# Kernel optimization log

Hardware: AMD Instinct MI355X
Metric: run time of the kernel (lower is better)

The kernel has to match this reference:

```python
import jax, jax.numpy as jnp
import numpy as np

C = 16
STRIDES = (8, 16, 32, 64, 128)
LVL_HW = ((256, 256), (128, 128), (64, 64), (32, 32), (16, 16))
K_POS = 256
K_HN = 2048
IOU_THRESH = 0.6
EPS = 1e-8


def _cross(a, b):
    return a[..., 0] * b[..., 1] - a[..., 1] * b[..., 0]


def _grid_points():
    # MlvlPointGenerator with offset=0.5: (x+0.5)*stride, row-major (y outer)
    pts, scl = [], []
    for lvl, ((h, w), s) in enumerate(zip(LVL_HW, STRIDES)):
        xs = (jnp.arange(w, dtype=jnp.float32) + 0.5) * s
        ys = (jnp.arange(h, dtype=jnp.float32) + 0.5) * s
        yy, xx = jnp.meshgrid(ys, xs, indexing='ij')
        pts.append(jnp.stack([xx.reshape(-1), yy.reshape(-1)], -1))
        scl.append(jnp.full((h * w,), float(lvl), dtype=jnp.float32))
    return jnp.concatenate(pts, 0), jnp.concatenate(scl, 0)


def _convert(cls_l, box_l, ang_l, ctr_l):
    B = cls_l[0].shape[0]
    cls = jnp.concatenate([x.transpose(0, 2, 3, 1).reshape(B, -1, C) for x in cls_l], 1).reshape(-1, C)
    box = jnp.concatenate([jnp.concatenate([b, a], 1).transpose(0, 2, 3, 1).reshape(B, -1, 5)
                           for b, a in zip(box_l, ang_l)], 1).reshape(-1, 5)
    ctr = jnp.concatenate([x.transpose(0, 2, 3, 1).reshape(B, -1, 1) for x in ctr_l], 1).reshape(-1, 1)
    return cls, box, ctr


def _decode(points, pred):  # DistanceAnglePointCoder.decode, angle_version='le90'
    l, t, r, b, a = [pred[..., i] for i in range(5)]
    ca, sa = jnp.cos(a), jnp.sin(a)
    w, h = l + r, t + b
    oxl, oyl = (r - l) * 0.5, (b - t) * 0.5
    ox = ca * oxl - sa * oyl
    oy = sa * oxl + ca * oyl
    an = (a + jnp.pi / 2) % jnp.pi - jnp.pi / 2
    return jnp.stack([points[..., 0] + ox, points[..., 1] + oy, w, h, an], -1)


def _encode(points, gt):  # DistanceAnglePointCoder.encode
    cx, cy, w, h, a = [gt[..., i] for i in range(5)]
    ca, sa = jnp.cos(a), jnp.sin(a)
    dx, dy = points[..., 0] - cx, points[..., 1] - cy
    ox = ca * dx + sa * dy
    oy = -sa * dx + ca * dy
    return jnp.stack([w / 2 + ox, h / 2 + oy, w / 2 - ox, h / 2 - oy, a], -1)


def _inside_mask(points, boxes):  # [M,2],[P,5] -> [M,P]
    cx, cy, w, h, a = [boxes[:, i][None, :] for i in range(5)]
    ca, sa = jnp.cos(a), jnp.sin(a)
    dx = points[:, 0:1] - cx
    dy = points[:, 1:2] - cy
    ox = ca * dx + sa * dy
    oy = -sa * dx + ca * dy
    m = jnp.minimum(jnp.minimum(w / 2 + ox, w / 2 - ox), jnp.minimum(h / 2 + oy, h / 2 - oy))
    return m > 0


def _corners(boxes):  # [N,5] -> [N,4,2]
    cx, cy, w, h, a = [boxes[:, i:i + 1] for i in range(5)]
    ca, sa = jnp.cos(a), jnp.sin(a)
    dx = jnp.array([-0.5, 0.5, 0.5, -0.5], jnp.float32) * w
    dy = jnp.array([-0.5, -0.5, 0.5, 0.5], jnp.float32) * h
    return jnp.stack([cx + dx * ca - dy * sa, cy + dx * sa + dy * ca], -1)


def _inter_area(ca, cb):  # intersection area of two convex quads [4,2],[4,2]
    pa, pb = ca, cb
    da = jnp.roll(ca, -1, 0) - ca
    db = jnp.roll(cb, -1, 0) - cb
    diff = pb[None, :] - pa[:, None]                     # [4,4,2]
    den = _cross(da[:, None], db[None, :])               # [4,4]
    dsafe = jnp.where(jnp.abs(den) < 1e-10, 1.0, den)
    t = _cross(diff, db[None, :]) / dsafe
    u = _cross(diff, da[:, None]) / dsafe
    ok = (jnp.abs(den) > 1e-10) & (t >= 0) & (t <= 1) & (u >= 0) & (u <= 1)
    ipts = pa[:, None] + t[..., None] * da[:, None]

    def inside(p, c):
        e = jnp.roll(c, -1, 0) - c
        s = _cross(e[None, :], p[:, None] - c[None, :])  # [4 pts, 4 edges]
        return jnp.all(s >= -1e-9, 1) | jnp.all(s <= 1e-9, 1)

    pts = jnp.concatenate([ipts.reshape(16, 2), ca, cb], 0)   # [24,2]
    val = jnp.concatenate([ok.reshape(16), inside(ca, cb), inside(cb, ca)], 0)
    n = val.sum()
    ctr = (pts * val[:, None]).sum(0) / jnp.maximum(n, 1)
    pts = jnp.where(val[:, None], pts, ctr)  # invalid pts collapse to centroid (zero area)
    order = jnp.argsort(jnp.arctan2(pts[:, 1] - ctr[1], pts[:, 0] - ctr[0]))
    pts = pts[order]
    area = 0.5 * jnp.abs(jnp.sum(_cross(pts - ctr, jnp.roll(pts, -1, 0) - ctr)))
    return jnp.where(n >= 3, area, 0.0)


def _rotated_iou(b1, b2):  # box_iou_rotated: [M,5],[P,5] -> [M,P]
    c1, c2 = _corners(b1), _corners(b2)
    inter = jax.vmap(lambda x: jax.vmap(lambda y: _inter_area(x, y))(c2))(c1)
    a1 = jnp.abs(b1[:, 2] * b1[:, 3])
    a2 = jnp.abs(b2[:, 2] * b2[:, 3])
    return inter / (a1[:, None] + a2[None, :] - inter + EPS)


def _bce(p, t):
    p = jnp.clip(p, 1e-12, 1.0 - 1e-12)
    return -(t * jnp.log(p) + (1.0 - t) * jnp.log1p(-p))


def _smooth_l1(x, y):  # nn.SmoothL1Loss(reduction='none'), beta=1
    d = jnp.abs(x - y)
    return jnp.where(d < 1.0, 0.5 * d * d, d - 0.5)


def _arsl_loss(t_cls, t_box, t_iou, s_cls, s_box, s_iou):
    # --- teacher targets (torch.no_grad) ---
    t_cls = jax.lax.stop_gradient(t_cls)
    t_box = jax.lax.stop_gradient(t_box)
    t_iou = jax.lax.stop_gradient(t_iou)
    points, scales = _grid_points()
    N = t_cls.shape[0]
    joint = jax.nn.sigmoid(t_cls) * jax.nn.sigmoid(t_iou)   # [N,C]
    max_vals = joint.max(-1)
    class_ind = joint.argmax(-1)
    cand = max_vals >= 0.1
    n_cand = cand.sum()
    mean = jnp.sum(max_vals * cand) / jnp.maximum(n_cand, 1)
    var = jnp.sum(cand * (max_vals - mean) ** 2) / jnp.maximum(n_cand - 1, 1)  # unbiased std
    pos_thresh = jnp.minimum(mean + jnp.sqrt(var), 0.4)
    pos_thresh = jnp.where(n_cand > 0, pos_thresh, jnp.inf)
    pos_mask = max_vals >= pos_thresh
    hn_mask = cand & (max_vals < pos_thresh)
    # fallback: top-10 positives when thresholding yields none
    fb = jnp.zeros((N,), bool).at[jax.lax.top_k(max_vals, 10)[1]].set(True)
    pos_mask = jnp.where(pos_mask.any(), pos_mask, fb)

    sig_t_cls = jax.nn.sigmoid(t_cls)
    sig_t_iou = jax.nn.sigmoid(t_iou[:, 0])
    cls_targets = jnp.where((pos_mask | hn_mask)[:, None], sig_t_cls, 0.0)
    loc_targets = jnp.where(pos_mask[:, None], t_box, 0.0)
    iou_targets = jnp.where(pos_mask, sig_t_iou, 0.0)
    loc_mask = pos_mask.astype(jnp.float32)

    # --- hard negative mining (fixed-capacity top-k selection) ---
    pv, pidx = jax.lax.top_k(jnp.where(pos_mask, max_vals, -1.0), K_POS)
    p_valid = jnp.take(pos_mask, pidx)
    _, hidx = jax.lax.top_k(jnp.where(hn_mask, max_vals, -1.0), K_HN)
    h_valid = jnp.take(hn_mask, hidx)
    pos_bbox = _decode(points[pidx], t_box[pidx])
    hn_pts = points[hidx]
    hn_bbox = _decode(hn_pts, t_box[hidx])
    iou = _rotated_iou(hn_bbox, pos_bbox)                    # [K_HN, K_POS]
    scale_flag = jnp.abs(scales[pidx][None, :] - scales[hidx][:, None]) <= 1.0
    class_flag = class_ind[pidx][None, :] == class_ind[hidx][:, None]
    inside_flag = _inside_mask(hn_pts, pos_bbox)
    valid = (iou >= IOU_THRESH) & class_flag & inside_flag & scale_flag & h_valid[:, None] & p_valid[None, :]
    iou_m = jnp.where(valid, iou, 0.0)
    potential = iou_m.max(-1) > 0.0                          # [K_HN]
    w = jnp.where(valid, pv[None, :], 0.0)                   # pos joint-confidence weights
    agg_bbox = (w[..., None] * pos_bbox[None]).sum(1) / jnp.maximum(w.sum(1), EPS)[:, None]
    agg_ltrba = _encode(hn_pts, agg_bbox)
    loc_targets = loc_targets.at[hidx].set(jnp.where(potential[:, None], agg_ltrba, loc_targets[hidx]))
    loc_mask = loc_mask.at[hidx].set(jnp.where(potential, 1.0, loc_mask[hidx]))

    loc_pos = loc_mask > 0.0
    iou_targets = jnp.where(loc_pos, sig_t_iou, iou_targets)
    cls_t_max = cls_targets.max(-1)
    cls_avg = jnp.sum(cls_t_max * pos_mask)
    loc_w = jnp.where(loc_pos, cls_t_max, 0.0)
    loc_avg = loc_w.sum()
    iou_avg = loc_pos.sum()

    # --- student losses ---
    s_cls_sig = jax.nn.sigmoid(s_cls)
    s_iou_sig = jax.nn.sigmoid(s_iou)
    jc = s_cls_sig * s_iou_sig  # quality focal loss on joint confidence, gamma=2
    loss_cls = jnp.sum(_bce(jc, cls_targets) * jnp.abs(jc - cls_targets) ** 2) / jnp.maximum(cls_avg, EPS)
    loss_iou = jnp.sum(_bce(s_iou_sig[:, 0], iou_targets) * loc_pos) / jnp.maximum(iou_avg, 1)
    loss_box = jnp.sum(_smooth_l1(s_box, loc_targets) * loc_w[:, None]) / jnp.maximum(loc_avg, EPS)
    return jnp.stack([loss_cls, loss_box, loss_iou])


def setup_inputs():
    key = jax.random.key(0)
    ks = jax.random.split(key, 10)
    inp = {}
    k = 0
    for pre in ('t', 's'):
        for i, (h, w) in enumerate(LVL_HW):
            k4 = jax.random.split(ks[k], 4); k += 1
            # sparse teacher/student confidences; positive box distances in image units
            inp[f'{pre}_cls_{i}'] = jax.random.normal(k4[0], (1, C, h, w), jnp.float32) * 3.0 - 12.0
            inp[f'{pre}_box_{i}'] = jax.random.uniform(k4[1], (1, 4, h, w), jnp.float32) * 64.0 + 1.0
            inp[f'{pre}_ang_{i}'] = jax.random.normal(k4[2], (1, 1, h, w), jnp.float32) * 0.5
            inp[f'{pre}_ctr_{i}'] = jax.random.normal(k4[3], (1, 1, h, w), jnp.float32)
    return inp


def reference(t_cls_0, t_cls_1, t_cls_2, t_cls_3, t_cls_4,
              t_box_0, t_box_1, t_box_2, t_box_3, t_box_4,
              t_ang_0, t_ang_1, t_ang_2, t_ang_3, t_ang_4,
              t_ctr_0, t_ctr_1, t_ctr_2, t_ctr_3, t_ctr_4,
              s_cls_0, s_cls_1, s_cls_2, s_cls_3, s_cls_4,
              s_box_0, s_box_1, s_box_2, s_box_3, s_box_4,
              s_ang_0, s_ang_1, s_ang_2, s_ang_3, s_ang_4,
              s_ctr_0, s_ctr_1, s_ctr_2, s_ctr_3, s_ctr_4):
    t = _convert([t_cls_0, t_cls_1, t_cls_2, t_cls_3, t_cls_4],
                 [t_box_0, t_box_1, t_box_2, t_box_3, t_box_4],
                 [t_ang_0, t_ang_1, t_ang_2, t_ang_3, t_ang_4],
                 [t_ctr_0, t_ctr_1, t_ctr_2, t_ctr_3, t_ctr_4])
    s = _convert([s_cls_0, s_cls_1, s_cls_2, s_cls_3, s_cls_4],
                 [s_box_0, s_box_1, s_box_2, s_box_3, s_box_4],
                 [s_ang_0, s_ang_1, s_ang_2, s_ang_3, s_ang_4],
                 [s_ctr_0, s_ctr_1, s_ctr_2, s_ctr_3, s_ctr_4])
    return _arsl_loss(t[0], t[1], t[2], s[0], s[1], s[2])
```

## Files before the change

kernel.cpp:

```cpp
#include <hip/hip_runtime.h>
#include <math.h>

#define NPTS 87296
#define NCLS 16
#define KPOS 256
#define KHN  2048
#define TILES 341
#define CAP  4096
#define PI_F   3.14159265358979323846f
#define HPI_F  1.57079632679489661923f

struct InPtrs { const float* p[40]; };

__device__ float g_max_vals[NPTS];
__device__ float g_sig_tiou[NPTS];
__device__ float g_sig_cls_max[NPTS];
__device__ int   g_class_ind[NPTS];
__device__ int   g_pos_mask[NPTS];
__device__ int   g_hn_mask[NPTS];
__device__ int   g_hnflag[NPTS];
__device__ float g_loc_targets[NPTS * 5];
__device__ float g_bsum[TILES];
__device__ float g_bsumsq[TILES];
__device__ int   g_bcnt[TILES];
__device__ int   g_bpos[TILES];
__device__ int   g_bhn[TILES];
__device__ float g_thresh;
__device__ int   g_tp, g_thn, g_slow;
__device__ int   g_pos_cand[CAP];
__device__ int   g_hn_cand[CAP];
__device__ int   g_pidx[KPOS];
__device__ int   g_pvalid[KPOS];
__device__ float g_pv[KPOS];
__device__ int   g_hidx[KHN];
__device__ int   g_hvalid[KHN];
__device__ float g_pos_bbox[KPOS * 5];
__device__ float g_pos_cor[KPOS * 8];
__device__ float g_pos_area[KPOS];
__device__ float g_pos_scale[KPOS];
__device__ int   g_pos_class[KPOS];
__device__ float g_hn_px[KHN];
__device__ float g_hn_py[KHN];
__device__ float g_hn_cor[KHN * 8];
__device__ float g_hn_area[KHN];
__device__ float g_hn_scale[KHN];
__device__ int   g_hn_class[KHN];
__device__ float g_partials[TILES * 6];

__device__ __forceinline__ float sigmoidf(float x) {
  if (x >= 0.f) return 1.f / (1.f + expf(-x));
  float e = expf(x);
  return e / (1.f + e);
}
__device__ __forceinline__ float crs(float ax, float ay, float bx, float by) {
  return ax * by - ay * bx;
}
__device__ __forceinline__ float mod_pos(float x, float y) {
  float r = fmodf(x, y);
  if (r < 0.f) r += y;
  return r;
}
__device__ __forceinline__ float pseudo_ang(float dx, float dy) {
  float den = fabsf(dx) + fabsf(dy);
  if (den == 0.f) return 0.f;
  return copysignf(1.f - dx / den, dy);
}
__device__ __forceinline__ void point_info(int n, int& lvl, int& idx, int& hw,
                                           float& px, float& py) {
  int off, wsh; float stride;
  if (n < 65536)      { lvl = 0; off = 0;     wsh = 8; stride = 8.f;   hw = 65536; }
  else if (n < 81920) { lvl = 1; off = 65536; wsh = 7; stride = 16.f;  hw = 16384; }
  else if (n < 86016) { lvl = 2; off = 81920; wsh = 6; stride = 32.f;  hw = 4096; }
  else if (n < 87040) { lvl = 3; off = 86016; wsh = 5; stride = 64.f;  hw = 1024; }
  else                { lvl = 4; off = 87040; wsh = 4; stride = 128.f; hw = 256; }
  idx = n - off;
  int y = idx >> wsh, x = idx & ((1 << wsh) - 1);
  px = ((float)x + 0.5f) * stride;
  py = ((float)y + 0.5f) * stride;
}

#define MASK_ALL 0
#define MASK_POS 1
#define MASK_HN  2
__device__ __forceinline__ int sel_mask(int mode, int n) {
  return mode == MASK_ALL ? 1 : (mode == MASK_POS ? g_pos_mask[n] : g_hn_mask[n]);
}

__device__ void radix_select_mask(int mode, int K, int* out_idx, int* out_valid, float* out_val,
                                  int* hist, int* scan_a, int* scan_b, int* sh) {
  int tid = threadIdx.x;
  int c = 0;
  for (int n = tid; n < NPTS; n += 256) if (sel_mask(mode, n)) c++;
  scan_a[tid] = c; __syncthreads();
  for (int st = 128; st > 0; st >>= 1) {
    if (tid < st) scan_a[tid] += scan_a[tid + st];
    __syncthreads();
  }
  int total = scan_a[0];
  __syncthreads();

  unsigned kth = 0u;
  if (total > K) {
    unsigned prefix = 0; int rem = K;
    for (int pass = 0; pass < 4; pass++) {
      int shift = 24 - 8 * pass;
      hist[tid] = 0;
      __syncthreads();
      for (int n = tid; n < NPTS; n += 256) {
        if (sel_mask(mode, n)) {
          unsigned k = __float_as_uint(g_max_vals[n]);
          if (pass == 0 || ((k >> (shift + 8)) == prefix))
            atomicAdd(&hist[(k >> shift) & 255], 1);
        }
      }
      __syncthreads();
      if (tid == 0) {
        int cum = 0, b = 255;
        for (; b > 0; b--) {
          if (cum + hist[b] >= rem) break;
          cum += hist[b];
        }
        sh[0] = (int)((prefix << 8) | (unsigned)b);
        sh[1] = rem - cum;
      }
      __syncthreads();
      prefix = (unsigned)sh[0]; rem = sh[1];
      __syncthreads();
    }
    kth = prefix;
  }

  const int chunk = (NPTS + 255) / 256;
  int start = tid * chunk; if (start > NPTS) start = NPTS;
  int end = start + chunk; if (end > NPTS) end = NPTS;
  int cgt = 0, ceq = 0;
  for (int n = start; n < end; n++) {
    if (sel_mask(mode, n)) {
      unsigned k = __float_as_uint(g_max_vals[n]);
      if (k > kth) cgt++;
      else if (k == kth) ceq++;
    }
  }
  scan_a[tid] = cgt; scan_b[tid] = ceq; __syncthreads();
  if (tid == 0) {
    int ag = 0, ae = 0;
    for (int i = 0; i < 256; i++) {
      int tg = scan_a[i], te = scan_b[i];
      scan_a[i] = ag; scan_b[i] = ae;
      ag += tg; ae += te;
    }
    sh[0] = ag; sh[1] = ae;
  }
  __syncthreads();
  int cnt_gt = sh[0], cnt_eq = sh[1];
  int og = scan_a[tid], oe = cnt_gt + scan_b[tid];
  for (int n = start; n < end; n++) {
    if (sel_mask(mode, n)) {
      unsigned k = __float_as_uint(g_max_vals[n]);
      if (k > kth) {
        out_idx[og] = n; out_valid[og] = 1;
        if (out_val) out_val[og] = g_max_vals[n];
        og++;
      } else if (k == kth) {
        if (oe < K) {
          out_idx[oe] = n; out_valid[oe] = 1;
          if (out_val) out_val[oe] = g_max_vals[n];
        }
        oe++;
      }
    }
  }
  int kmc = K - cnt_gt;
  int used = cnt_gt + (cnt_eq < kmc ? cnt_eq : kmc);
  __syncthreads();
  for (int i = used + tid; i < K; i += 256) {
    out_idx[i] = 0; out_valid[i] = 0;
    if (out_val) out_val[i] = -1.f;
  }
  __syncthreads();
}

__device__ void radix_select_list(const int* list, int count, int K,
                                  int* out_idx, int* out_valid, float* out_val,
                                  int* hist, int* scan_a, int* scan_b, int* sh) {
  int tid = threadIdx.x;
  unsigned prefix = 0; int rem = K;
  for (int pass = 0; pass < 4; pass++) {
    int shift = 24 - 8 * pass;
    hist[tid] = 0;
    __syncthreads();
    for (int i = tid; i < count; i += 256) {
      unsigned k = __float_as_uint(g_max_vals[list[i]]);
      if (pass == 0 || ((k >> (shift + 8)) == prefix))
        atomicAdd(&hist[(k >> shift) & 255], 1);
    }
    __syncthreads();
    if (tid == 0) {
      int cum = 0, b = 255;
      for (; b > 0; b--) {
        if (cum + hist[b] >= rem) break;
        cum += hist[b];
      }
      sh[0] = (int)((prefix << 8) | (unsigned)b);
      sh[1] = rem - cum;
    }
    __syncthreads();
    prefix = (unsigned)sh[0]; rem = sh[1];
    __syncthreads();
  }
  unsigned kth = prefix;
  int chunk = (count + 255) / 256;
  int start = tid * chunk; if (start > count) start = count;
  int end = start + chunk; if (end > count) end = count;
  int cgt = 0, ceq = 0;
  for (int i = start; i < end; i++) {
    unsigned k = __float_as_uint(g_max_vals[list[i]]);
    if (k > kth) cgt++;
    else if (k == kth) ceq++;
  }
  scan_a[tid] = cgt; scan_b[tid] = ceq; __syncthreads();
  if (tid == 0) {
    int ag = 0, ae = 0;
    for (int i = 0; i < 256; i++) {
      int tg = scan_a[i], te = scan_b[i];
      scan_a[i] = ag; scan_b[i] = ae;
      ag += tg; ae += te;
    }
    sh[0] = ag;
  }
  __syncthreads();
  int cnt_gt = sh[0];
  int og = scan_a[tid], oe = cnt_gt + scan_b[tid];
  for (int i = start; i < end; i++) {
    int n = list[i];
    unsigned k = __float_as_uint(g_max_vals[n]);
    if (k > kth) {
      out_idx[og] = n; out_valid[og] = 1;
      if (out_val) out_val[og] = g_max_vals[n];
      og++;
    } else if (k == kth) {
      if (oe < K) {
        out_idx[oe] = n; out_valid[oe] = 1;
        if (out_val) out_val[oe] = g_max_vals[n];
      }
      oe++;
    }
  }
  __syncthreads();
}

__device__ void decode_box(int n, const InPtrs& P, float* bb, float* cor,
                           float& area, float& scale, int& cls_out,
                           float* opx, float* opy) {
  int lvl, idx, hw; float px, py;
  point_info(n, lvl, idx, hw, px, py);
  const float* box = P.p[lvl * 4 + 1];
  const float* ang = P.p[lvl * 4 + 2];
  float l = box[idx], t = box[hw + idx], r = box[2 * hw + idx], b = box[3 * hw + idx];
  float a = ang[idx];
  float ca = cosf(a), sa = sinf(a);
  float w = l + r, h = t + b;
  float oxl = (r - l) * 0.5f, oyl = (b - t) * 0.5f;
  float ox = ca * oxl - sa * oyl;
  float oy = sa * oxl + ca * oyl;
  float an = mod_pos(a + HPI_F, PI_F) - HPI_F;
  float cx = px + ox, cy = py + oy;
  bb[0] = cx; bb[1] = cy; bb[2] = w; bb[3] = h; bb[4] = an;
  float c2 = cosf(an), s2 = sinf(an);
  const float dxs[4] = {-0.5f, 0.5f, 0.5f, -0.5f};
  const float dys[4] = {-0.5f, -0.5f, 0.5f, 0.5f};
#pragma unroll
  for (int k = 0; k < 4; k++) {
    float dx = dxs[k] * w, dy = dys[k] * h;
    cor[2 * k]     = cx + dx * c2 - dy * s2;
    cor[2 * k + 1] = cy + dx * s2 + dy * c2;
  }
  area = fabsf(w * h);
  scale = (float)lvl;
  cls_out = g_class_ind[n];
  if (opx) { *opx = px; *opy = py; }
}

__device__ void decode_to_pos_slot(int o, int n, const InPtrs& P) {
  float bb[5], cor[8], ar, sc; int cl;
  decode_box(n, P, bb, cor, ar, sc, cl, (float*)0, (float*)0);
#pragma unroll
  for (int k = 0; k < 5; k++) g_pos_bbox[o * 5 + k] = bb[k];
#pragma unroll
  for (int k = 0; k < 8; k++) g_pos_cor[o * 8 + k] = cor[k];
  g_pos_area[o] = ar; g_pos_scale[o] = sc; g_pos_class[o] = cl;
  g_pv[o] = g_max_vals[n];
}
__device__ void decode_to_hn_slot(int o, int n, const InPtrs& P) {
  float bb[5], cor[8], ar, sc, px, py; int cl;
  decode_box(n, P, bb, cor, ar, sc, cl, &px, &py);
#pragma unroll
  for (int k = 0; k < 8; k++) g_hn_cor[o * 8 + k] = cor[k];
  g_hn_area[o] = ar; g_hn_scale[o] = sc; g_hn_class[o] = cl;
  g_hn_px[o] = px; g_hn_py[o] = py;
}

#define BPASS(KK, JJ)                                                      \
  _Pragma("unroll")                                                        \
  for (int i = 0; i < 32; i++) {                                           \
    int l = i ^ (JJ);                                                      \
    if (l > i) {                                                           \
      bool up = ((i & (KK)) == 0);                                         \
      float aa = sa_[i], ab = sa_[l];                                      \
      bool sw = up ? (aa > ab) : (aa < ab);                                \
      sa_[i] = sw ? ab : aa; sa_[l] = sw ? aa : ab;                        \
      float xi = sx_[i], xl = sx_[l];                                      \
      sx_[i] = sw ? xl : xi; sx_[l] = sw ? xi : xl;                        \
      float yi = sy_[i], yl = sy_[l];                                      \
      sy_[i] = sw ? yl : yi; sy_[l] = sw ? yi : yl;                        \
    }                                                                      \
  }

__device__ float inter_area(const float* __restrict__ A, const float* __restrict__ B) {
  float ax[4], ay[4], bx[4], by[4];
#pragma unroll
  for (int i = 0; i < 4; i++) {
    ax[i] = A[2 * i]; ay[i] = A[2 * i + 1];
    bx[i] = B[2 * i]; by[i] = B[2 * i + 1];
  }
  float dax[4], day[4], dbx[4], dby[4];
#pragma unroll
  for (int i = 0; i < 4; i++) {
    int i1 = (i + 1) & 3;
    dax[i] = ax[i1] - ax[i]; day[i] = ay[i1] - ay[i];
    dbx[i] = bx[i1] - bx[i]; dby[i] = by[i1] - by[i];
  }
  float px[24], py[24]; bool val[24];
#pragma unroll
  for (int i = 0; i < 4; i++) {
#pragma unroll
    for (int j = 0; j < 4; j++) {
      float dx = bx[j] - ax[i], dy = by[j] - ay[i];
      float den = crs(dax[i], day[i], dbx[j], dby[j]);
      float ad = fabsf(den);
      float ds = (ad < 1e-10f) ? 1.0f : den;
      float t = crs(dx, dy, dbx[j], dby[j]) / ds;
      float u = crs(dx, dy, dax[i], day[i]) / ds;
      bool ok = (ad > 1e-10f) & (t >= 0.f) & (t <= 1.f) & (u >= 0.f) & (u <= 1.f);
      int k = i * 4 + j;
      px[k] = ax[i] + t * dax[i];
      py[k] = ay[i] + t * day[i];
      val[k] = ok;
    }
  }
#pragma unroll
  for (int i = 0; i < 4; i++) {
    bool ge = true, le = true;
#pragma unroll
    for (int j = 0; j < 4; j++) {
      float s = crs(dbx[j], dby[j], ax[i] - bx[j], ay[i] - by[j]);
      ge = ge && (s >= -1e-9f);
      le = le && (s <= 1e-9f);
    }
    val[16 + i] = ge || le; px[16 + i] = ax[i]; py[16 + i] = ay[i];
  }
#pragma unroll
  for (int j = 0; j < 4; j++) {
    bool ge = true, le = true;
#pragma unroll
    for (int i = 0; i < 4; i++) {
      float s = crs(dax[i], day[i], bx[j] - ax[i], by[j] - ay[i]);
      ge = ge && (s >= -1e-9f);
      le = le && (s <= 1e-9f);
    }
    val[20 + j] = ge || le; px[20 + j] = bx[j]; py[20 + j] = by[j];
  }
  int n = 0; float sx = 0.f, sy = 0.f;
#pragma unroll
  for (int k = 0; k < 24; k++) if (val[k]) { n++; sx += px[k]; sy += py[k]; }
  float dn = (float)(n > 1 ? n : 1);
  float cx = sx / dn, cy = sy / dn;

  float sa_[32], sx_[32], sy_[32];
#pragma unroll
  for (int k = 0; k < 24; k++) {
    float X = val[k] ? px[k] : cx;
    float Y = val[k] ? py[k] : cy;
    sx_[k] = X; sy_[k] = Y;
    sa_[k] = pseudo_ang(X - cx, Y - cy);
  }
#pragma unroll
  for (int k = 24; k < 32; k++) {
    sa_[k] = __int_as_float(0x7f800000);
    sx_[k] = cx; sy_[k] = cy;
  }
  BPASS(2, 1)
  BPASS(4, 2)  BPASS(4, 1)
  BPASS(8, 4)  BPASS(8, 2)  BPASS(8, 1)
  BPASS(16, 8) BPASS(16, 4) BPASS(16, 2) BPASS(16, 1)
  BPASS(32, 16) BPASS(32, 8) BPASS(32, 4) BPASS(32, 2) BPASS(32, 1)

  float s2 = 0.f;
#pragma unroll
  for (int k = 0; k < 24; k++) {
    int k1 = (k + 1) % 24;
    s2 += crs(sx_[k] - cx, sy_[k] - cy, sx_[k1] - cx, sy_[k1] - cy);
  }
  float area = 0.5f * fabsf(s2);
  return (n >= 3) ? area : 0.f;
}

__global__ __launch_bounds__(256) void k_prep(InPtrs P) {
  int tid = threadIdx.x;
  int t = blockIdx.x;
  int n = t * 256 + tid;
  __shared__ float r0[256], r1[256], r2[256];

  int lvl, idx, hw; float px, py;
  point_info(n, lvl, idx, hw, px, py);
  const float* cls = P.p[lvl * 4 + 0];
  const float* ctr = P.p[lvl * 4 + 3];
  float stiou = sigmoidf(ctr[idx]);
  float mv = -1.f, scm = 0.f; int ci = 0;
  for (int c = 0; c < NCLS; c++) {
    float sc = sigmoidf(cls[c * hw + idx]);
    if (sc > scm) scm = sc;
    float j = sc * stiou;
    if (j > mv) { mv = j; ci = c; }
  }
  g_max_vals[n] = mv;
  g_class_ind[n] = ci;
  g_sig_tiou[n] = stiou;
  g_sig_cls_max[n] = scm;
  g_hnflag[n] = 0;
  float isc = (mv >= 0.1f) ? 1.f : 0.f;
  r0[tid] = isc; r1[tid] = isc * mv; r2[tid] = isc * mv * mv;
  __syncthreads();
  for (int st = 128; st > 0; st >>= 1) {
    if (tid < st) { r0[tid] += r0[tid + st]; r1[tid] += r1[tid + st]; r2[tid] += r2[tid + st]; }
    __syncthreads();
  }
  if (tid == 0) {
    g_bcnt[t] = (int)r0[0];
    g_bsum[t] = r1[0];
    g_bsumsq[t] = r2[0];
  }
}

__global__ __launch_bounds__(256) void k_mask() {
  int tid = threadIdx.x;
  int t = blockIdx.x;
  int n = t * 256 + tid;
  __shared__ float s1[256], s2[256];
  __shared__ int s0[256];
  int c = 0; float s = 0.f, q = 0.f;
  for (int i = tid; i < TILES; i += 256) { c += g_bcnt[i]; s += g_bsum[i]; q += g_bsumsq[i]; }
  s0[tid] = c; s1[tid] = s; s2[tid] = q; __syncthreads();
  for (int st = 128; st > 0; st >>= 1) {
    if (tid < st) { s0[tid] += s0[tid + st]; s1[tid] += s1[tid + st]; s2[tid] += s2[tid + st]; }
    __syncthreads();
  }
  int nc = s0[0]; float sum = s1[0], sumsq = s2[0];
  float mean = sum / (float)(nc > 1 ? nc : 1);
  float E = sumsq - 2.f * mean * sum + (float)nc * mean * mean;
  if (E < 0.f) E = 0.f;
  float var = E / (float)((nc - 1) > 1 ? (nc - 1) : 1);
  float th = fminf(mean + sqrtf(var), 0.4f);
  if (nc == 0) th = __int_as_float(0x7f800000);
  if (t == 0 && tid == 0) g_thresh = th;

  float v = g_max_vals[n];
  int pm = (v >= th) ? 1 : 0;
  int hm = (v >= 0.1f && v < th) ? 1 : 0;
  g_pos_mask[n] = pm; g_hn_mask[n] = hm;
  __syncthreads();
  __shared__ int t0[256], t1[256];
  t0[tid] = pm; t1[tid] = hm; __syncthreads();
  for (int st = 128; st > 0; st >>= 1) {
    if (tid < st) { t0[tid] += t0[tid + st]; t1[tid] += t1[tid + st]; }
    __syncthreads();
  }
  if (tid == 0) { g_bpos[t] = t0[0]; g_bhn[t] = t1[0]; }
}

__global__ __launch_bounds__(256) void k_compact(InPtrs P) {
  int tid = threadIdx.x;
  int t = blockIdx.x;
  int n = t * 256 + tid;
  __shared__ int si0[256], si1[256];

  int cp = 0, ch = 0;
  for (int i = tid; i < t; i += 256) { cp += g_bpos[i]; ch += g_bhn[i]; }
  si0[tid] = cp; si1[tid] = ch; __syncthreads();
  for (int st = 128; st > 0; st >>= 1) {
    if (tid < st) { si0[tid] += si0[tid + st]; si1[tid] += si1[tid + st]; }
    __syncthreads();
  }
  int poff = si0[0], hoff = si1[0];
  __syncthreads();

  int pm = g_pos_mask[n], hm = g_hn_mask[n];
  si0[tid] = pm; si1[tid] = hm; __syncthreads();
  for (int off = 1; off < 256; off <<= 1) {
    int ap = (tid >= off) ? si0[tid - off] : 0;
    int ah = (tid >= off) ? si1[tid - off] : 0;
    __syncthreads();
    si0[tid] += ap; si1[tid] += ah;
    __syncthreads();
  }
  if (pm) {
    int o = poff + si0[tid] - pm;
    if (o < CAP) g_pos_cand[o] = n;
    if (o < KPOS) decode_to_pos_slot(o, n, P);
  }
  if (hm) {
    int o = hoff + si1[tid] - hm;
    if (o < CAP) g_hn_cand[o] = n;
    if (o < KHN) decode_to_hn_slot(o, n, P);
  }
  if (t == TILES - 1 && tid == 255) {
    int tp = poff + si0[255];
    int thn = hoff + si1[255];
    g_tp = tp; g_thn = thn;
    g_slow = (tp == 0 || tp > KPOS || thn > KHN) ? 1 : 0;
  }
}

__global__ __launch_bounds__(256) void k_select(InPtrs P) {
  if (!g_slow) return;
  __shared__ int hist[256], si0[256], si1[256], sh_i[2];
  int tid = threadIdx.x;
  int tp = g_tp, thn = g_thn;
  int fallback = (tp == 0) ? 1 : 0;
  if (!fallback && tp <= KPOS) {
    for (int i = tid; i < KPOS; i += 256) {
      if (i < tp) {
        int m = g_pos_cand[i];
        g_pidx[i] = m; g_pvalid[i] = 1; g_pv[i] = g_max_vals[m];
      } else { g_pidx[i] = 0; g_pvalid[i] = 0; g_pv[i] = -1.f; }
    }
    __syncthreads();
  } else if (!fallback && tp <= CAP) {
    radix_select_list(g_pos_cand, tp, KPOS, g_pidx, g_pvalid, g_pv, hist, si0, si1, sh_i);
  } else if (!fallback) {
    radix_select_mask(MASK_POS, KPOS, g_pidx, g_pvalid, g_pv, hist, si0, si1, sh_i);
  } else {
    radix_select_mask(MASK_ALL, 10, g_pidx, g_pvalid, g_pv, hist, si0, si1, sh_i);
    for (int i = tid; i < 10; i += 256)
      if (g_pvalid[i]) g_pos_mask[g_pidx[i]] = 1;
    for (int i = 10 + tid; i < KPOS; i += 256) {
      g_pidx[i] = 0; g_pvalid[i] = 0; g_pv[i] = -1.f;
    }
    __syncthreads();
  }
  if (thn <= KHN) {
    for (int i = tid; i < KHN; i += 256) {
      if (i < thn) { g_hidx[i] = g_hn_cand[i]; g_hvalid[i] = 1; }
      else { g_hidx[i] = 0; g_hvalid[i] = 0; }
    }
  } else if (thn <= CAP) {
    radix_select_list(g_hn_cand, thn, KHN, g_hidx, g_hvalid, (float*)0, hist, si0, si1, sh_i);
  } else {
    radix_select_mask(MASK_HN, KHN, g_hidx, g_hvalid, (float*)0, hist, si0, si1, sh_i);
  }
  __syncthreads();
  for (int i = tid; i < KPOS; i += 256)
    if (g_pvalid[i]) { decode_to_pos_slot(i, g_pidx[i], P); }
  for (int i = tid; i < KHN; i += 256)
    if (g_hvalid[i]) { decode_to_hn_slot(i, g_hidx[i], P); }
}

__global__ __launch_bounds__(256) void k_iou() {
  const int h = blockIdx.x;
  const int j = threadIdx.x;
  const int slow = g_slow;
  const int tp = g_tp, thn = g_thn;

  const int hv = slow ? g_hvalid[h] : ((h < thn) ? 1 : 0);
  if (!hv) return;
  const int nh = slow ? g_hidx[h] : g_hn_cand[h];

  float hcor[8];
#pragma unroll
  for (int k = 0; k < 8; k++) hcor[k] = g_hn_cor[h * 8 + k];
  const float har = g_hn_area[h], hsc = g_hn_scale[h];
  const float hpx = g_hn_px[h], hpy = g_hn_py[h];
  const int hcl = g_hn_class[h];

  const int pvld = slow ? g_pvalid[j] : ((j < tp) ? 1 : 0);
  bool pre = false;
  if (pvld) {
    pre = (g_pos_class[j] == hcl) && (fabsf(g_pos_scale[j] - hsc) <= 1.0f);
    if (pre) {
      float cx = g_pos_bbox[j * 5 + 0], cy = g_pos_bbox[j * 5 + 1];
      float bw = g_pos_bbox[j * 5 + 2], bh = g_pos_bbox[j * 5 + 3];
      float an = g_pos_bbox[j * 5 + 4];
      float ca = cosf(an), sa = sinf(an);
      float dx = hpx - cx, dy = hpy - cy;
      float ox = ca * dx + sa * dy, oy = -sa * dx + ca * dy;
      float mm = fminf(fminf(bw * 0.5f + ox, bw * 0.5f - ox),
                       fminf(bh * 0.5f + oy, bh * 0.5f - oy));
      pre = (mm > 0.f);
    }
  }

  __shared__ int lst[256], scn[256];
  __shared__ float rw[7][256];
  scn[j] = pre ? 1 : 0;
#pragma unroll
  for (int k = 0; k < 7; k++) rw[k][j] = 0.f;
  __syncthreads();
  for (int off = 1; off < 256; off <<= 1) {
    int a = (j >= off) ? scn[j - off] : 0;
    __syncthreads();
    scn[j] += a;
    __syncthreads();
  }
  if (pre) lst[scn[j] - 1] = j;
  int nv = scn[255];
  __syncthreads();

  for (int i = j; i < nv; i += 256) {
    int jj = lst[i];
    float pcor[8];
#pragma unroll
    for (int k = 0; k < 8; k++) pcor[k] = g_pos_cor[jj * 8 + k];
    float inter = inter_area(hcor, pcor);
    float iou = inter / (har + g_pos_area[jj] - inter + 1e-8f);
    if (iou >= 0.6f) {
      float pv = g_pv[jj];
      rw[0][jj] = pv;
#pragma unroll
      for (int k = 0; k < 5; k++) rw[1 + k][jj] = pv * g_pos_bbox[jj * 5 + k];
      rw[6][jj] = 1.f;
    }
  }
  __syncthreads();
  for (int st = 128; st > 0; st >>= 1) {
    if (j < st)
#pragma unroll
      for (int k = 0; k < 7; k++) rw[k][j] += rw[k][j + st];
    __syncthreads();
  }
  if (j == 0 && rw[6][0] > 0.f) {
    float inv = 1.f / fmaxf(rw[0][0], 1e-8f);
    float bb[5];
#pragma unroll
    for (int k = 0; k < 5; k++) bb[k] = rw[1 + k][0] * inv;
    float ca = cosf(bb[4]), sa = sinf(bb[4]);
    float dx = hpx - bb[0], dy = hpy - bb[1];
    float ox = ca * dx + sa * dy, oy = -sa * dx + ca * dy;
    g_loc_targets[nh * 5 + 0] = bb[2] * 0.5f + ox;
    g_loc_targets[nh * 5 + 1] = bb[3] * 0.5f + oy;
    g_loc_targets[nh * 5 + 2] = bb[2] * 0.5f - ox;
    g_loc_targets[nh * 5 + 3] = bb[3] * 0.5f - oy;
    g_loc_targets[nh * 5 + 4] = bb[4];
    g_hnflag[nh] = 1;
  }
}

__global__ __launch_bounds__(256) void k_loss(InPtrs P) {
  int tid = threadIdx.x;
  int t = blockIdx.x;
  int n = t * 256 + tid;
  __shared__ float red[6][256];
  float v0, v1, v2, v3, v4, v5;
  {
    int lvl, idx, hw; float px, py;
    point_info(n, lvl, idx, hw, px, py);
    int pm = g_pos_mask[n], hm = g_hn_mask[n], hf = g_hnflag[n];
    int sel = pm | hm;
    bool lp = (pm | hf) != 0;
    float ctmax = sel ? g_sig_cls_max[n] : 0.f;
    const float* tcls = P.p[lvl * 4 + 0];
    const float* tbox = P.p[lvl * 4 + 1];
    const float* tang = P.p[lvl * 4 + 2];
    const float* scls = P.p[20 + lvl * 4 + 0];
    const float* sbox = P.p[20 + lvl * 4 + 1];
    const float* sang = P.p[20 + lvl * 4 + 2];
    const float* sctr = P.p[20 + lvl * 4 + 3];
    float siou = sigmoidf(sctr[idx]);
    float scl = 0.f;
    for (int c = 0; c < NCLS; c++) {
      float jc = sigmoidf(scls[c * hw + idx]) * siou;
      float ct = sel ? sigmoidf(tcls[c * hw + idx]) : 0.f;
      float p = jc;
      if (p < 1e-12f) p = 1e-12f;
      float pu = 1.f - 1e-12f;
      if (p > pu) p = pu;
      float bce = -(ct * logf(p) + (1.f - ct) * log1pf(-p));
      float d = fabsf(jc - ct);
      scl += bce * d * d;
    }
    v0 = scl;
    float lw = lp ? ctmax : 0.f;
    float tgt[5];
    if (hf) {
#pragma unroll
      for (int k = 0; k < 5; k++) tgt[k] = g_loc_targets[n * 5 + k];
    } else if (pm) {
      tgt[0] = tbox[idx]; tgt[1] = tbox[hw + idx];
      tgt[2] = tbox[2 * hw + idx]; tgt[3] = tbox[3 * hw + idx];
      tgt[4] = tang[idx];
    } else {
#pragma unroll
      for (int k = 0; k < 5; k++) tgt[k] = 0.f;
    }
    float sb = 0.f;
#pragma unroll
    for (int k = 0; k < 5; k++) {
      float sv = (k < 4) ? sbox[k * hw + idx] : sang[idx];
      float d = fabsf(sv - tgt[k]);
      sb += (d < 1.f) ? 0.5f * d * d : d - 0.5f;
    }
    v1 = sb * lw;
    v2 = 0.f;
    if (lp) {
      float p = siou;
      if (p < 1e-12f) p = 1e-12f;
      float pu = 1.f - 1e-12f;
      if (p > pu) p = pu;
      float ti = g_sig_tiou[n];
      v2 = -(ti * logf(p) + (1.f - ti) * log1pf(-p));
    }
    v3 = pm ? ctmax : 0.f;
    v4 = lw;
    v5 = lp ? 1.f : 0.f;
  }
  red[0][tid] = v0; red[1][tid] = v1; red[2][tid] = v2;
  red[3][tid] = v3; red[4][tid] = v4; red[5][tid] = v5;
  __syncthreads();
  for (int st = 128; st > 0; st >>= 1) {
    if (tid < st)
#pragma unroll
      for (int k = 0; k < 6; k++) red[k][tid] += red[k][tid + st];
    __syncthreads();
  }
  if (tid == 0)
#pragma unroll
    for (int k = 0; k < 6; k++) g_partials[t * 6 + k] = red[k][0];
}

__global__ __launch_bounds__(256) void k_final(float* out) {
  int tid = threadIdx.x;
  float a[6] = {0,0,0,0,0,0};
  for (int b = tid; b < TILES; b += 256)
#pragma unroll
    for (int k = 0; k < 6; k++) a[k] += g_partials[b * 6 + k];
  __shared__ float red[6][256];
#pragma unroll
  for (int k = 0; k < 6; k++) red[k][tid] = a[k];
  __syncthreads();
  for (int st = 128; st > 0; st >>= 1) {
    if (tid < st)
#pragma unroll
      for (int k = 0; k < 6; k++) red[k][tid] += red[k][tid + st];
    __syncthreads();
  }
  if (tid == 0) {
    out[0] = red[0][0] / fmaxf(red[3][0], 1e-8f);
    out[1] = red[1][0] / fmaxf(red[4][0], 1e-8f);
    out[2] = red[2][0] / fmaxf(red[5][0], 1.f);
  }
}

extern "C" void kernel_launch(void* const* d_in, const int* in_sizes, int n_in,
                              void* d_out, int out_size, void* d_ws, size_t ws_size,
                              hipStream_t stream) {
  (void)in_sizes; (void)n_in; (void)out_size; (void)d_ws; (void)ws_size;
  InPtrs P;
  for (int i = 0; i < 40; i++) P.p[i] = (const float*)d_in[i];
  k_prep<<<TILES, 256, 0, stream>>>(P);
  k_mask<<<TILES, 256, 0, stream>>>();
  k_compact<<<TILES, 256, 0, stream>>>(P);
  k_select<<<1, 256, 0, stream>>>(P);
  k_iou<<<KHN, 256, 0, stream>>>();
  k_loss<<<TILES, 256, 0, stream>>>(P);
  k_final<<<1, 256, 0, stream>>>((float*)d_out);
}
```

Before: 54.57 us.

## Fold slow-path select kernel into IoU kernel with per-block redundant selection

Removes the single-block k_select launch by having every k_iou block redo the slow-path top-k selection in LDS and decode its boxes locally. On the fast path this saves one kernel launch and its global-memory traffic. The cost is a much larger shared-memory footprint in k_iou (about 15 KB more LDS per block), which may lower occupancy, plus heavily redundant work across 2048 blocks whenever the slow path is taken. The global index and valid arrays are dropped.

```diff
diff --git a/kernel.cpp b/kernel.cpp
--- a/kernel.cpp
+++ b/kernel.cpp
@@ -29,16 +29,12 @@
 __device__ int   g_tp, g_thn, g_slow;
 __device__ int   g_pos_cand[CAP];
 __device__ int   g_hn_cand[CAP];
-__device__ int   g_pidx[KPOS];
-__device__ int   g_pvalid[KPOS];
-__device__ float g_pv[KPOS];
-__device__ int   g_hidx[KHN];
-__device__ int   g_hvalid[KHN];
 __device__ float g_pos_bbox[KPOS * 5];
 __device__ float g_pos_cor[KPOS * 8];
 __device__ float g_pos_area[KPOS];
 __device__ float g_pos_scale[KPOS];
 __device__ int   g_pos_class[KPOS];
+__device__ float g_pv[KPOS];
 __device__ float g_hn_px[KHN];
 __device__ float g_hn_py[KHN];
 __device__ float g_hn_cor[KHN * 8];
@@ -247,6 +243,43 @@
     }
   }
   __syncthreads();
+}
+
+__device__ void slow_select_lds(int tp, int thn, int fallback,
+                                int* s_pidx, int* s_pvalid, float* s_pv,
+                                int* s_hidx, int* s_hvalid,
+                                int* hist, int* scan_a, int* scan_b, int* sh_i) {
+  int tid = threadIdx.x;
+  if (!fallback && tp <= KPOS) {
+    for (int i = tid; i < KPOS; i += 256) {
+      if (i < tp) {
+        int m = g_pos_cand[i];
+        s_pidx[i] = m; s_pvalid[i] = 1; s_pv[i] = g_max_vals[m];
+      } else { s_pidx[i] = 0; s_pvalid[i] = 0; s_pv[i] = -1.f; }
+    }
+    __syncthreads();
+  } else if (!fallback && tp <= CAP) {
+    radix_select_list(g_pos_cand, tp, KPOS, s_pidx, s_pvalid, s_pv, hist, scan_a, scan_b, sh_i);
+  } else if (!fallback) {
+    radix_select_mask(MASK_POS, KPOS, s_pidx, s_pvalid, s_pv, hist, scan_a, scan_b, sh_i);
+  } else {
+    radix_select_mask(MASK_ALL, 10, s_pidx, s_pvalid, s_pv, hist, scan_a, scan_b, sh_i);
+    for (int i = 10 + tid; i < KPOS; i += 256) {
+      s_pidx[i] = 0; s_pvalid[i] = 0; s_pv[i] = -1.f;
+    }
+    __syncthreads();
+  }
+  if (thn <= KHN) {
+    for (int i = tid; i < KHN; i += 256) {
+      if (i < thn) { s_hidx[i] = g_hn_cand[i]; s_hvalid[i] = 1; }
+      else { s_hidx[i] = 0; s_hvalid[i] = 0; }
+    }
+    __syncthreads();
+  } else if (thn <= CAP) {
+    radix_select_list(g_hn_cand, thn, KHN, s_hidx, s_hvalid, (float*)0, hist, scan_a, scan_b, sh_i);
+  } else {
+    radix_select_mask(MASK_HN, KHN, s_hidx, s_hvalid, (float*)0, hist, scan_a, scan_b, sh_i);
+  }
 }
 
 __device__ void decode_box(int n, const InPtrs& P, float* bb, float* cor,
@@ -521,116 +554,127 @@
   }
 }
 
-__global__ __launch_bounds__(256) void k_select(InPtrs P) {
-  if (!g_slow) return;
-  __shared__ int hist[256], si0[256], si1[256], sh_i[2];
-  int tid = threadIdx.x;
-  int tp = g_tp, thn = g_thn;
-  int fallback = (tp == 0) ? 1 : 0;
-  if (!fallback && tp <= KPOS) {
-    for (int i = tid; i < KPOS; i += 256) {
-      if (i < tp) {
-        int m = g_pos_cand[i];
-        g_pidx[i] = m; g_pvalid[i] = 1; g_pv[i] = g_max_vals[m];
-      } else { g_pidx[i] = 0; g_pvalid[i] = 0; g_pv[i] = -1.f; }
-    }
-    __syncthreads();
-  } else if (!fallback && tp <= CAP) {
-    radix_select_list(g_pos_cand, tp, KPOS, g_pidx, g_pvalid, g_pv, hist, si0, si1, sh_i);
-  } else if (!fallback) {
-    radix_select_mask(MASK_POS, KPOS, g_pidx, g_pvalid, g_pv, hist, si0, si1, sh_i);
-  } else {
-    radix_select_mask(MASK_ALL, 10, g_pidx, g_pvalid, g_pv, hist, si0, si1, sh_i);
-    for (int i = tid; i < 10; i += 256)
-      if (g_pvalid[i]) g_pos_mask[g_pidx[i]] = 1;
-    for (int i = 10 + tid; i < KPOS; i += 256) {
-      g_pidx[i] = 0; g_pvalid[i] = 0; g_pv[i] = -1.f;
-    }
-    __syncthreads();
-  }
-  if (thn <= KHN) {
-    for (int i = tid; i < KHN; i += 256) {
-      if (i < thn) { g_hidx[i] = g_hn_cand[i]; g_hvalid[i] = 1; }
-      else { g_hidx[i] = 0; g_hvalid[i] = 0; }
-    }
-  } else if (thn <= CAP) {
-    radix_select_list(g_hn_cand, thn, KHN, g_hidx, g_hvalid, (float*)0, hist, si0, si1, sh_i);
-  } else {
-    radix_select_mask(MASK_HN, KHN, g_hidx, g_hvalid, (float*)0, hist, si0, si1, sh_i);
-  }
-  __syncthreads();
-  for (int i = tid; i < KPOS; i += 256)
-    if (g_pvalid[i]) { decode_to_pos_slot(i, g_pidx[i], P); }
-  for (int i = tid; i < KHN; i += 256)
-    if (g_hvalid[i]) { decode_to_hn_slot(i, g_hidx[i], P); }
-}
-
-__global__ __launch_bounds__(256) void k_iou() {
+__global__ __launch_bounds__(256) void k_iou(InPtrs P) {
   const int h = blockIdx.x;
   const int j = threadIdx.x;
   const int slow = g_slow;
   const int tp = g_tp, thn = g_thn;
 
-  const int hv = slow ? g_hvalid[h] : ((h < thn) ? 1 : 0);
-  if (!hv) return;
-  const int nh = slow ? g_hidx[h] : g_hn_cand[h];
-
-  float hcor[8];
-#pragma unroll
-  for (int k = 0; k < 8; k++) hcor[k] = g_hn_cor[h * 8 + k];
-  const float har = g_hn_area[h], hsc = g_hn_scale[h];
-  const float hpx = g_hn_px[h], hpy = g_hn_py[h];
-  const int hcl = g_hn_class[h];
-
-  const int pvld = slow ? g_pvalid[j] : ((j < tp) ? 1 : 0);
-  bool pre = false;
-  if (pvld) {
-    pre = (g_pos_class[j] == hcl) && (fabsf(g_pos_scale[j] - hsc) <= 1.0f);
-    if (pre) {
-      float cx = g_pos_bbox[j * 5 + 0], cy = g_pos_bbox[j * 5 + 1];
-      float bw = g_pos_bbox[j * 5 + 2], bh = g_pos_bbox[j * 5 + 3];
-      float an = g_pos_bbox[j * 5 + 4];
-      float ca = cosf(an), sa = sinf(an);
-      float dx = hpx - cx, dy = hpy - cy;
-      float ox = ca * dx + sa * dy, oy = -sa * dx + ca * dy;
-      float mm = fminf(fminf(bw * 0.5f + ox, bw * 0.5f - ox),
-                       fminf(bh * 0.5f + oy, bh * 0.5f - oy));
-      pre = (mm > 0.f);
-    }
-  }
-
+  __shared__ float rw[7][256];
   __shared__ int lst[256], scn[256];
-  __shared__ float rw[7][256];
-  scn[j] = pre ? 1 : 0;
-#pragma unroll
-  for (int k = 0; k < 7; k++) rw[k][j] = 0.f;
-  __syncthreads();
-  for (int off = 1; off < 256; off <<= 1) {
-    int a = (j >= off) ? scn[j - off] : 0;
-    __syncthreads();
-    scn[j] += a;
-    __syncthreads();
-  }
-  if (pre) lst[scn[j] - 1] = j;
-  int nv = scn[255];
-  __syncthreads();
-
-  for (int i = j; i < nv; i += 256) {
-    int jj = lst[i];
-    float pcor[8];
-#pragma unroll
-    for (int k = 0; k < 8; k++) pcor[k] = g_pos_cor[jj * 8 + k];
-    float inter = inter_area(hcor, pcor);
-    float iou = inter / (har + g_pos_area[jj] - inter + 1e-8f);
-    if (iou >= 0.6f) {
-      float pv = g_pv[jj];
-      rw[0][jj] = pv;
-#pragma unroll
-      for (int k = 0; k < 5; k++) rw[1 + k][jj] = pv * g_pos_bbox[jj * 5 + k];
-      rw[6][jj] = 1.f;
-    }
-  }
-  __syncthreads();
+  __shared__ int   s_pidx[KPOS], s_pvalid[KPOS];
+  __shared__ float s_pv[KPOS];
+  __shared__ int   s_hidx[KHN], s_hvalid[KHN];
+  __shared__ int   hist[256], sca[256], scb[256], sh_i[2];
+
+  int nh;
+  float hcor[8], har, hsc, hpx, hpy; int hcl;
+
+  if (!slow) {
+    const int hv = (h < thn) ? 1 : 0;
+    if (!hv) return;
+    nh = g_hn_cand[h];
+#pragma unroll
+    for (int k = 0; k < 8; k++) hcor[k] = g_hn_cor[h * 8 + k];
+    har = g_hn_area[h]; hsc = g_hn_scale[h];
+    hpx = g_hn_px[h]; hpy = g_hn_py[h];
+    hcl = g_hn_class[h];
+
+    const int pvld = (j < tp) ? 1 : 0;
+    bool pre = false;
+    if (pvld) {
+      pre = (g_pos_class[j] == hcl) && (fabsf(g_pos_scale[j] - hsc) <= 1.0f);
+      if (pre) {
+        float cx = g_pos_bbox[j * 5 + 0], cy = g_pos_bbox[j * 5 + 1];
+        float bw = g_pos_bbox[j * 5 + 2], bh = g_pos_bbox[j * 5 + 3];
+        float an = g_pos_bbox[j * 5 + 4];
+        float ca = cosf(an), sa = sinf(an);
+        float dx = hpx - cx, dy = hpy - cy;
+        float ox = ca * dx + sa * dy, oy = -sa * dx + ca * dy;
+        float mm = fminf(fminf(bw * 0.5f + ox, bw * 0.5f - ox),
+                         fminf(bh * 0.5f + oy, bh * 0.5f - oy));
+        pre = (mm > 0.f);
+      }
+    }
+
+    scn[j] = pre ? 1 : 0;
+#pragma unroll
+    for (int k = 0; k < 7; k++) rw[k][j] = 0.f;
+    __syncthreads();
+    for (int off = 1; off < 256; off <<= 1) {
+      int a = (j >= off) ? scn[j - off] : 0;
+      __syncthreads();
+      scn[j] += a;
+      __syncthreads();
+    }
+    if (pre) lst[scn[j] - 1] = j;
+    int nv = scn[255];
+    __syncthreads();
+
+    for (int i = j; i < nv; i += 256) {
+      int jj = lst[i];
+      float pcor[8];
+#pragma unroll
+      for (int k = 0; k < 8; k++) pcor[k] = g_pos_cor[jj * 8 + k];
+      float inter = inter_area(hcor, pcor);
+      float iou = inter / (har + g_pos_area[jj] - inter + 1e-8f);
+      if (iou >= 0.6f) {
+        float pv = g_pv[jj];
+        rw[0][jj] = pv;
+#pragma unroll
+        for (int k = 0; k < 5; k++) rw[1 + k][jj] = pv * g_pos_bbox[jj * 5 + k];
+        rw[6][jj] = 1.f;
+      }
+    }
+    __syncthreads();
+  } else {
+    const int fallback = (tp == 0) ? 1 : 0;
+    slow_select_lds(tp, thn, fallback, s_pidx, s_pvalid, s_pv, s_hidx, s_hvalid,
+                    hist, sca, scb, sh_i);
+    if (fallback && h == 0) {
+      for (int i = j; i < 10; i += 256)
+        if (s_pvalid[i]) g_pos_mask[s_pidx[i]] = 1;
+    }
+    const int hv = s_hvalid[h];
+    if (!hv) return;
+    nh = s_hidx[h];
+    {
+      float hbb[5]; float ar, sc; int cl;
+      decode_box(nh, P, hbb, hcor, ar, sc, cl, &hpx, &hpy);
+      har = ar; hsc = sc; hcl = cl;
+    }
+#pragma unroll
+    for (int k = 0; k < 7; k++) rw[k][j] = 0.f;
+    __syncthreads();
+    if (s_pvalid[j]) {
+      int m = s_pidx[j];
+      float pv = s_pv[j];
+      float pbb[5], pcor[8], par, psc; int pcl;
+      decode_box(m, P, pbb, pcor, par, psc, pcl, (float*)0, (float*)0);
+      bool valid = (pcl == hcl) && (fabsf(psc - hsc) <= 1.0f);
+      if (valid) {
+        float ca = cosf(pbb[4]), sa = sinf(pbb[4]);
+        float dx = hpx - pbb[0], dy = hpy - pbb[1];
+        float ox = ca * dx + sa * dy, oy = -sa * dx + ca * dy;
+        float mm = fminf(fminf(pbb[2] * 0.5f + ox, pbb[2] * 0.5f - ox),
+                         fminf(pbb[3] * 0.5f + oy, pbb[3] * 0.5f - oy));
+        valid = (mm > 0.f);
+      }
+      if (valid) {
+        float inter = inter_area(hcor, pcor);
+        float iou = inter / (har + par - inter + 1e-8f);
+        valid = (iou >= 0.6f);
+      }
+      if (valid) {
+        rw[0][j] = pv;
+#pragma unroll
+        for (int k = 0; k < 5; k++) rw[1 + k][j] = pv * pbb[k];
+        rw[6][j] = 1.f;
+      }
+    }
+    __syncthreads();
+  }
+
   for (int st = 128; st > 0; st >>= 1) {
     if (j < st)
 #pragma unroll
@@ -768,8 +812,7 @@
   k_prep<<<TILES, 256, 0, stream>>>(P);
   k_mask<<<TILES, 256, 0, stream>>>();
   k_compact<<<TILES, 256, 0, stream>>>(P);
-  k_select<<<1, 256, 0, stream>>>(P);
-  k_iou<<<KHN, 256, 0, stream>>>();
+  k_iou<<<KHN, 256, 0, stream>>>(P);
   k_loss<<<TILES, 256, 0, stream>>>(P);
   k_final<<<1, 256, 0, stream>>>((float*)d_out);
 }
```

After: 55.13 us. Within noise of the previous version (+1.0%).
